# Kernel tuning notes

Hardware: AMD Instinct MI355X
Metric: run time of the kernel (lower is better)

## Reference

```python
import jax, jax.numpy as jnp
import numpy as np

RES, K, H = 8192, 48, 128

def _layer_norm(x, g, b, eps=1e-5):
    mu = jnp.mean(x, axis=-1, keepdims=True)
    var = jnp.var(x, axis=-1, keepdims=True)
    return (x - mu) * jax.lax.rsqrt(var + eps) * g + b

def _gelu(x):
    return jax.nn.gelu(x, approximate=False)  # torch default exact GELU

def setup_inputs() -> dict:
    key = jax.random.key(0)
    ks = jax.random.split(key, 16)
    s = 0.05
    inp = {
        "node_h": jax.random.normal(ks[0], (RES, H), jnp.float32),
        "edge_h": jax.random.normal(ks[1], (RES, K, H), jnp.float32),
        "edge_idx": jax.random.randint(ks[2], (RES, K), 0, RES, jnp.int32),
        "seq_emb": jax.random.normal(ks[3], (RES, H), jnp.float32),
        "ar_mask": jax.random.uniform(ks[4], (RES, K), jnp.float32),
        # msg_mlp: Linear(4h,h) -> GELU -> Linear(h,h) -> GELU -> Linear(h,h)
        "mW1": jax.random.normal(ks[5], (4 * H, H), jnp.float32) * s,
        "mb1": jnp.zeros((H,), jnp.float32),
        "mW2": jax.random.normal(ks[6], (H, H), jnp.float32) * s,
        "mb2": jnp.zeros((H,), jnp.float32),
        "mW3": jax.random.normal(ks[7], (H, H), jnp.float32) * s,
        "mb3": jnp.zeros((H,), jnp.float32),
        # ff_node: Linear(h,4h) -> GELU -> Linear(4h,h)
        "fW1": jax.random.normal(ks[8], (H, 4 * H), jnp.float32) * s,
        "fb1": jnp.zeros((4 * H,), jnp.float32),
        "fW2": jax.random.normal(ks[9], (4 * H, H), jnp.float32) * s,
        "fb2": jnp.zeros((H,), jnp.float32),
        "g1": jnp.ones((H,), jnp.float32), "b1": jnp.zeros((H,), jnp.float32),
        "g2": jnp.ones((H,), jnp.float32), "b2": jnp.zeros((H,), jnp.float32),
    }
    return inp

def reference(node_h, edge_h, edge_idx, seq_emb, ar_mask,
              mW1, mb1, mW2, mb2, mW3, mb3,
              fW1, fb1, fW2, fb2, g1, b1, g2, b2):
    seq_j = seq_emb[edge_idx] * ar_mask[..., None]           # [res,k,h]
    e_dec = jnp.concatenate([edge_h, seq_j], axis=-1)        # [res,k,2h]
    h_j = node_h[edge_idx]                                   # [res,k,h]
    h_i = jnp.broadcast_to(node_h[:, None, :], (node_h.shape[0], edge_idx.shape[1], node_h.shape[1]))
    x = jnp.concatenate([h_i, h_j, e_dec], axis=-1)          # [res,k,4h]
    msg = _gelu(x @ mW1 + mb1)
    msg = _gelu(msg @ mW2 + mb2)
    msg = msg @ mW3 + mb3                                    # [res,k,h]
    agg = jnp.sum(msg, axis=1)                               # [res,h]
    h = _layer_norm(node_h + agg, g1, b1)
    ff = _gelu(h @ fW1 + fb1) @ fW2 + fb2
    h = _layer_norm(h + ff, g2, b2)
    return h
```

## Files before the change

### kernel.cpp

```cpp
#include <hip/hip_runtime.h>

#define KNB 48

typedef float  floatx4 __attribute__((ext_vector_type(4)));
typedef __bf16 bf16x8  __attribute__((ext_vector_type(8)));
typedef unsigned short ushort8  __attribute__((ext_vector_type(8)));
typedef unsigned short ushort4v __attribute__((ext_vector_type(4)));

__device__ __forceinline__ float bf2f(unsigned short b) {
  union { unsigned int u; float f; } v; v.u = ((unsigned int)b) << 16; return v.f;
}
__device__ __forceinline__ unsigned short f2bf(float f) {
  __bf16 h = (__bf16)f;
  union { __bf16 h; unsigned short u; } v; v.h = h; return v.u;
}
__device__ __forceinline__ float gelu_f(float x) {
  float u = x * (0.7978845608f + 0.0356774081f * x * x);
  float t = __builtin_amdgcn_exp2f(u * -2.8853900818f);
  return x * __builtin_amdgcn_rcpf(1.0f + t);
}

__global__ __launch_bounds__(256) void k0_transpose(
    const float* mW1, const float* mW2, const float* mW3,
    const float* fW1, const float* fW2,
    unsigned short* MT1, unsigned short* WT2, unsigned short* WT3,
    unsigned short* FWT1, unsigned short* FWT2) {
  __shared__ unsigned short tile[32][33];
  int b = blockIdx.x;
  const float* src; unsigned short* dst; int Kd, Nd, t;
  if (b < 64)       { src = mW1; dst = MT1;  Kd = 512; Nd = 128; t = b; }
  else if (b < 80)  { src = mW2; dst = WT2;  Kd = 128; Nd = 128; t = b - 64; }
  else if (b < 96)  { src = mW3; dst = WT3;  Kd = 128; Nd = 128; t = b - 80; }
  else if (b < 160) { src = fW1; dst = FWT1; Kd = 128; Nd = 512; t = b - 96; }
  else              { src = fW2; dst = FWT2; Kd = 512; Nd = 128; t = b - 160; }
  int tN = Nd >> 5;
  int tk = t / tN, tn = t % tN;
  int tx = threadIdx.x & 31, ty = threadIdx.x >> 5;
  for (int r = 0; r < 4; ++r) {
    int row = ty + r * 8;
    tile[row][tx] = f2bf(src[(size_t)(tk * 32 + row) * Nd + tn * 32 + tx]);
  }
  __syncthreads();
  for (int r = 0; r < 4; ++r) {
    int row = ty + r * 8;
    dst[(size_t)(tn * 32 + row) * Kd + tk * 32 + tx] = tile[tx][row];
  }
}

__global__ __launch_bounds__(256) void k1_nodepre(
    const float* node_h, const float* seq_emb,
    const unsigned short* MT1, const float* mb1,
    float* Apr, unsigned short* BS) {
  __shared__ __align__(16) unsigned short sX[2][32 * 128];
  int r0 = blockIdx.x * 32;
  int tid = threadIdx.x, lane = tid & 63, w = tid >> 6;
  int l15 = lane & 15, l16 = lane >> 4;

  for (int mset = 0; mset < 2; ++mset) {
    const float* src = mset ? (seq_emb + (size_t)r0 * 128) : (node_h + (size_t)r0 * 128);
    for (int k = 0; k < 4; ++k) {
      int f = tid + 256 * k;
      floatx4 v = ((const floatx4*)src)[f];
      int row = f >> 5, hc = f & 31, c = hc >> 1, half = hc & 1;
      ushort4v o;
      o[0] = f2bf(v[0]); o[1] = f2bf(v[1]); o[2] = f2bf(v[2]); o[3] = f2bf(v[3]);
      *(ushort4v*)((char*)&sX[mset][0] + row * 256 + ((c ^ (row & 7)) << 4) + half * 8) = o;
    }
  }
  __syncthreads();

  for (int q = 0; q < 6; ++q) {
    int job = w + 4 * q;
    int kind = job >> 3;
    int nt = job & 7;
    int colOff = (kind == 0) ? 0 : (kind == 1) ? 128 : 384;
    const unsigned short* X = sX[kind == 2 ? 1 : 0];
    bf16x8 wf[4];
    for (int kk = 0; kk < 4; ++kk)
      wf[kk] = *(const bf16x8*)(MT1 + (size_t)(nt * 16 + l15) * 512 + colOff + kk * 32 + l16 * 8);
    for (int mt = 0; mt < 2; ++mt) {
      floatx4 acc = {0.f, 0.f, 0.f, 0.f};
      for (int kk = 0; kk < 4; ++kk) {
        int row = mt * 16 + l15;
        int off = (kk * 64 + l16 * 16) ^ ((row & 7) << 4);
        bf16x8 a = *(const bf16x8*)((const char*)X + row * 256 + off);
        acc = __builtin_amdgcn_mfma_f32_16x16x32_bf16(a, wf[kk], acc, 0, 0, 0);
      }
      int col = nt * 16 + l15;
      for (int r = 0; r < 4; ++r) {
        int row = r0 + mt * 16 + l16 * 4 + r;
        if (kind == 0)      Apr[(size_t)row * 128 + col] = acc[r] + mb1[col];
        else if (kind == 1) BS[(size_t)row * 256 + col] = f2bf(acc[r]);
        else                BS[(size_t)row * 256 + 128 + col] = f2bf(acc[r]);
      }
    }
  }
}

__global__ __launch_bounds__(512, 8) void k2_edge(
    const float* edge_h, const int* edge_idx, const float* ar_mask,
    const unsigned short* MT1, const unsigned short* WT2, const unsigned short* WT3,
    const float* mb2, const float* mb3,
    const float* Apr, const unsigned short* BS,
    float* agg) {
  __shared__ __align__(16) unsigned short sE[48 * 128];
  __shared__ __align__(16) unsigned short sT[48 * 128];
  int i0 = blockIdx.x;
  int tid = threadIdx.x, lane = tid & 63, w = tid >> 6;
  int l15 = lane & 15, l16 = lane >> 4;
  int rb = (l16 & 1) * 4;
  int colw = w * 16 + l15;
  int cp = ((colw >> 3) << 4) | ((l15 & 7) << 1);

  const float* eb = edge_h + (size_t)i0 * KNB * 128;
#pragma unroll
  for (int k = 0; k < 3; ++k) {
    int f = tid + 512 * k;
    floatx4 v = ((const floatx4*)eb)[f];
    int row = f >> 5, hc = f & 31, c = hc >> 1, half = hc & 1;
    ushort4v o;
    o[0] = f2bf(v[0]); o[1] = f2bf(v[1]); o[2] = f2bf(v[2]); o[3] = f2bf(v[3]);
    *(ushort4v*)((char*)sE + row * 256 + ((c ^ (row & 7)) << 4) + half * 8) = o;
  }
  for (int u = tid; u < 48 * 16; u += 512) {
    int e = u >> 4, c8 = u & 15;
    int j = edge_idx[(size_t)i0 * KNB + e];
    float m = ar_mask[(size_t)i0 * KNB + e];
    const floatx4* ap = (const floatx4*)(Apr + (size_t)i0 * 128 + c8 * 8);
    floatx4 a0 = ap[0], a1 = ap[1];
    ushort8 vb = *(const ushort8*)(BS + (size_t)j * 256 + c8 * 8);
    ushort8 vs = *(const ushort8*)(BS + (size_t)j * 256 + 128 + c8 * 8);
    ushort8 res;
#pragma unroll
    for (int x = 0; x < 4; ++x)
      res[x] = f2bf(a0[x] + bf2f(vb[x]) + m * bf2f(vs[x]));
#pragma unroll
    for (int x = 0; x < 4; ++x)
      res[4 + x] = f2bf(a1[x] + bf2f(vb[4 + x]) + m * bf2f(vs[4 + x]));
    *(ushort8*)((char*)sT + e * 256 + ((c8 ^ (e & 7)) * 16)) = res;
  }
  __syncthreads();

  {
    bf16x8 wf[4];
#pragma unroll
    for (int kk = 0; kk < 4; ++kk)
      wf[kk] = *(const bf16x8*)(MT1 + (size_t)colw * 512 + 256 + kk * 32 + l16 * 8);
#pragma unroll
    for (int mt = 0; mt < 3; ++mt) {
      floatx4 acc = {0.f,0.f,0.f,0.f};
#pragma unroll
      for (int kk = 0; kk < 4; ++kk) {
        int row = mt * 16 + l15;
        int off = (kk * 64 + l16 * 16) ^ ((row & 7) << 4);
        bf16x8 a = *(const bf16x8*)((const char*)sE + row * 256 + off);
        acc = __builtin_amdgcn_mfma_f32_16x16x32_bf16(a, wf[kk], acc, 0, 0, 0);
      }
      char* base = (char*)sT + (mt * 16 + l16 * 4) * 256;
#pragma unroll
      for (int r = 0; r < 4; ++r) {
        char* p = base + r * 256 + (cp ^ ((rb + r) << 4));
        float g = bf2f(*(unsigned short*)p);
        *(unsigned short*)p = f2bf(gelu_f(acc[r] + g));
      }
    }
  }
  __syncthreads();

  {
    bf16x8 wf[4];
#pragma unroll
    for (int kk = 0; kk < 4; ++kk)
      wf[kk] = *(const bf16x8*)(WT2 + (size_t)colw * 128 + kk * 32 + l16 * 8);
    float bb = mb2[colw];
#pragma unroll
    for (int mt = 0; mt < 3; ++mt) {
      floatx4 acc = {0.f,0.f,0.f,0.f};
#pragma unroll
      for (int kk = 0; kk < 4; ++kk) {
        int row = mt * 16 + l15;
        int off = (kk * 64 + l16 * 16) ^ ((row & 7) << 4);
        bf16x8 a = *(const bf16x8*)((const char*)sT + row * 256 + off);
        acc = __builtin_amdgcn_mfma_f32_16x16x32_bf16(a, wf[kk], acc, 0, 0, 0);
      }
      char* base = (char*)sE + (mt * 16 + l16 * 4) * 256;
#pragma unroll
      for (int r = 0; r < 4; ++r) {
        char* p = base + r * 256 + (cp ^ ((rb + r) << 4));
        *(unsigned short*)p = f2bf(gelu_f(acc[r] + bb));
      }
    }
  }
  __syncthreads();

  {
    bf16x8 wf[4];
#pragma unroll
    for (int kk = 0; kk < 4; ++kk)
      wf[kk] = *(const bf16x8*)(WT3 + (size_t)colw * 128 + kk * 32 + l16 * 8);
    float agga[4] = {0.f,0.f,0.f,0.f};
#pragma unroll
    for (int mt = 0; mt < 3; ++mt) {
      floatx4 acc = {0.f,0.f,0.f,0.f};
#pragma unroll
      for (int kk = 0; kk < 4; ++kk) {
        int row = mt * 16 + l15;
        int off = (kk * 64 + l16 * 16) ^ ((row & 7) << 4);
        bf16x8 a = *(const bf16x8*)((const char*)sE + row * 256 + off);
        acc = __builtin_amdgcn_mfma_f32_16x16x32_bf16(a, wf[kk], acc, 0, 0, 0);
      }
#pragma unroll
      for (int r = 0; r < 4; ++r) agga[r] += acc[r];
    }
    float s = agga[0] + agga[1] + agga[2] + agga[3];
    s += __shfl_xor(s, 16);
    s += __shfl_xor(s, 32);
    if (lane < 16) {
      int col = w * 16 + lane;
      agg[(size_t)i0 * 128 + col] = s + 48.0f * mb3[col];
    }
  }
}

__global__ __launch_bounds__(256) void k3_ff(
    const float* node_h, const float* agg,
    const unsigned short* FWT1, const unsigned short* FWT2,
    const float* fb1, const float* fb2,
    const float* g1, const float* b1,
    const float* g2, const float* b2,
    float* out) {
  __shared__ __align__(16) unsigned short sH[32 * 128];
  __shared__ __align__(16) unsigned short sT3[32 * 512];
  __shared__ float sP[32 * 128];
  int r0 = blockIdx.x * 32;
  int tid = threadIdx.x, lane = tid & 63, w = tid >> 6;
  int l15 = lane & 15, l16 = lane >> 4;

  {
    int row = tid >> 3;
    int c0 = (tid & 7) * 16;
    const floatx4* nh4 = (const floatx4*)(node_h + (size_t)(r0 + row) * 128 + c0);
    const floatx4* ag4 = (const floatx4*)(agg + (size_t)(r0 + row) * 128 + c0);
    float x[16]; float sum = 0.f, sum2 = 0.f;
#pragma unroll
    for (int q4 = 0; q4 < 4; ++q4) {
      floatx4 a = nh4[q4], g = ag4[q4];
#pragma unroll
      for (int j = 0; j < 4; ++j) {
        float xv = a[j] + g[j];
        x[q4 * 4 + j] = xv; sum += xv; sum2 += xv * xv;
      }
    }
    sum  += __shfl_xor(sum, 1);  sum  += __shfl_xor(sum, 2);  sum  += __shfl_xor(sum, 4);
    sum2 += __shfl_xor(sum2, 1); sum2 += __shfl_xor(sum2, 2); sum2 += __shfl_xor(sum2, 4);
    float mu = sum * (1.f / 128.f);
    float var = sum2 * (1.f / 128.f) - mu * mu;
    float rstd = rsqrtf(var + 1e-5f);
#pragma unroll
    for (int q = 0; q < 16; ++q) {
      int col = c0 + q;
      float h = (x[q] - mu) * rstd * g1[col] + b1[col];
      sP[row * 128 + col] = h;
      char* p = (char*)sH + row * 256 + ((((col >> 3) ^ (row & 7)) << 4) | ((col & 7) << 1));
      *(unsigned short*)p = f2bf(h);
    }
  }
  __syncthreads();

  for (int nq = 0; nq < 8; ++nq) {
    int nt = w * 8 + nq;
    bf16x8 wf[4];
    for (int kk = 0; kk < 4; ++kk)
      wf[kk] = *(const bf16x8*)(FWT1 + (size_t)(nt * 16 + l15) * 128 + kk * 32 + l16 * 8);
    for (int mt = 0; mt < 2; ++mt) {
      floatx4 acc = {0.f,0.f,0.f,0.f};
      for (int kk = 0; kk < 4; ++kk) {
        int row = mt * 16 + l15;
        int off = (kk * 64 + l16 * 16) ^ ((row & 7) << 4);
        bf16x8 a = *(const bf16x8*)((const char*)sH + row * 256 + off);
        acc = __builtin_amdgcn_mfma_f32_16x16x32_bf16(a, wf[kk], acc, 0, 0, 0);
      }
      int col = nt * 16 + l15;
      float bb = fb1[col];
      for (int r = 0; r < 4; ++r) {
        int row = mt * 16 + l16 * 4 + r;
        char* p = (char*)sT3 + row * 1024 + ((((col >> 3) ^ (row & 7)) << 4) | ((col & 7) << 1));
        *(unsigned short*)p = f2bf(gelu_f(acc[r] + bb));
      }
    }
  }
  __syncthreads();

  for (int n = 0; n < 2; ++n) {
    int nt = 2 * w + n;
    for (int mt = 0; mt < 2; ++mt) {
      floatx4 acc = {0.f,0.f,0.f,0.f};
      for (int kk = 0; kk < 16; ++kk) {
        int row = mt * 16 + l15;
        int off = (kk * 64 + l16 * 16) ^ ((row & 7) << 4);
        bf16x8 a = *(const bf16x8*)((const char*)sT3 + row * 1024 + off);
        bf16x8 b = *(const bf16x8*)(FWT2 + (size_t)(nt * 16 + l15) * 512 + kk * 32 + l16 * 8);
        acc = __builtin_amdgcn_mfma_f32_16x16x32_bf16(a, b, acc, 0, 0, 0);
      }
      int col = nt * 16 + l15;
      float bb = fb2[col];
      for (int r = 0; r < 4; ++r) {
        int row = mt * 16 + l16 * 4 + r;
        sP[row * 128 + col] += acc[r] + bb;
      }
    }
  }
  __syncthreads();

  {
    int row = tid >> 3;
    int c0 = (tid & 7) * 16;
    float x[16]; float sum = 0.f, sum2 = 0.f;
#pragma unroll
    for (int q = 0; q < 16; ++q) {
      float xv = sP[row * 128 + c0 + q];
      x[q] = xv; sum += xv; sum2 += xv * xv;
    }
    sum  += __shfl_xor(sum, 1);  sum  += __shfl_xor(sum, 2);  sum  += __shfl_xor(sum, 4);
    sum2 += __shfl_xor(sum2, 1); sum2 += __shfl_xor(sum2, 2); sum2 += __shfl_xor(sum2, 4);
    float mu = sum * (1.f / 128.f);
    float var = sum2 * (1.f / 128.f) - mu * mu;
    float rstd = rsqrtf(var + 1e-5f);
#pragma unroll
    for (int q = 0; q < 16; ++q) {
      int col = c0 + q;
      out[(size_t)(r0 + row) * 128 + col] = (x[q] - mu) * rstd * g2[col] + b2[col];
    }
  }
}

extern "C" void kernel_launch(void* const* d_in, const int* in_sizes, int n_in,
                              void* d_out, int out_size, void* d_ws, size_t ws_size,
                              hipStream_t stream) {
  const float* node_h  = (const float*)d_in[0];
  const float* edge_h  = (const float*)d_in[1];
  const int*   edge_idx= (const int*)d_in[2];
  const float* seq_emb = (const float*)d_in[3];
  const float* ar_mask = (const float*)d_in[4];
  const float* mW1 = (const float*)d_in[5];
  const float* mb1 = (const float*)d_in[6];
  const float* mW2 = (const float*)d_in[7];
  const float* mb2 = (const float*)d_in[8];
  const float* mW3 = (const float*)d_in[9];
  const float* mb3 = (const float*)d_in[10];
  const float* fW1 = (const float*)d_in[11];
  const float* fb1 = (const float*)d_in[12];
  const float* fW2 = (const float*)d_in[13];
  const float* fb2 = (const float*)d_in[14];
  const float* g1  = (const float*)d_in[15];
  const float* b1  = (const float*)d_in[16];
  const float* g2  = (const float*)d_in[17];
  const float* b2  = (const float*)d_in[18];

  char* ws = (char*)d_ws;
  unsigned short* MT1  = (unsigned short*)(ws + 0);
  unsigned short* WT2  = (unsigned short*)(ws + 131072);
  unsigned short* WT3  = (unsigned short*)(ws + 163840);
  unsigned short* FWT1 = (unsigned short*)(ws + 196608);
  unsigned short* FWT2 = (unsigned short*)(ws + 327680);
  float*          Apr  = (float*)(ws + 458752);
  unsigned short* BS   = (unsigned short*)(ws + 4653056);
  float*          agg  = (float*)(ws + 8847360);

  hipLaunchKernelGGL(k0_transpose, dim3(224), dim3(256), 0, stream,
                     mW1, mW2, mW3, fW1, fW2, MT1, WT2, WT3, FWT1, FWT2);
  hipLaunchKernelGGL(k1_nodepre, dim3(256), dim3(256), 0, stream,
                     node_h, seq_emb, MT1, mb1, Apr, BS);
  hipLaunchKernelGGL(k2_edge, dim3(8192), dim3(512), 0, stream,
                     edge_h, edge_idx, ar_mask, MT1, WT2, WT3, mb2, mb3,
                     Apr, BS, agg);
  hipLaunchKernelGGL(k3_ff, dim3(256), dim3(256), 0, stream,
                     node_h, agg, FWT1, FWT2, fb1, fb2, g1, b1, g2, b2,
                     (float*)d_out);
}
```

Measured before the change: 156.6 us.

## Map one wavefront per node in edge MLP kernel, removing block barriers

The edge-MLP kernel now gives each wavefront one whole node: a 256-thread block handles four nodes, and each wave has its own shared-memory tile. Edge features are loaded straight from global memory into MFMA A-fragments held in registers. Each wave computes all 8 column tiles for its node, so the block-wide __syncthreads between layers go away and the edge_h staging copy is dropped. The cost is a much higher register count (A-fragments plus three accumulators), fewer waves per block, and weight fragments being reloaded for every column tile in every wave.

```diff
diff --git a/kernel.cpp b/kernel.cpp
--- a/kernel.cpp
+++ b/kernel.cpp
@@ -14,11 +14,19 @@
   __bf16 h = (__bf16)f;
   union { __bf16 h; unsigned short u; } v; v.h = h; return v.u;
 }
+__device__ __forceinline__ bf16x8 pack8(floatx4 a, floatx4 b) {
+  bf16x8 r;
+  r[0] = (__bf16)a[0]; r[1] = (__bf16)a[1]; r[2] = (__bf16)a[2]; r[3] = (__bf16)a[3];
+  r[4] = (__bf16)b[0]; r[5] = (__bf16)b[1]; r[6] = (__bf16)b[2]; r[7] = (__bf16)b[3];
+  return r;
+}
 __device__ __forceinline__ float gelu_f(float x) {
   float u = x * (0.7978845608f + 0.0356774081f * x * x);
   float t = __builtin_amdgcn_exp2f(u * -2.8853900818f);
   return x * __builtin_amdgcn_rcpf(1.0f + t);
 }
+
+#define MFMA16(a, b, c) __builtin_amdgcn_mfma_f32_16x16x32_bf16((a), (b), (c), 0, 0, 0)
 
 __global__ __launch_bounds__(256) void k0_transpose(
     const float* mW1, const float* mW2, const float* mW3,
@@ -84,7 +92,7 @@
         int row = mt * 16 + l15;
         int off = (kk * 64 + l16 * 16) ^ ((row & 7) << 4);
         bf16x8 a = *(const bf16x8*)((const char*)X + row * 256 + off);
-        acc = __builtin_amdgcn_mfma_f32_16x16x32_bf16(a, wf[kk], acc, 0, 0, 0);
+        acc = MFMA16(a, wf[kk], acc);
       }
       int col = nt * 16 + l15;
       for (int r = 0; r < 4; ++r) {
@@ -97,127 +105,156 @@
   }
 }
 
-__global__ __launch_bounds__(512, 8) void k2_edge(
+__global__ __launch_bounds__(256, 3) void k2_edge(
     const float* edge_h, const int* edge_idx, const float* ar_mask,
     const unsigned short* MT1, const unsigned short* WT2, const unsigned short* WT3,
     const float* mb2, const float* mb3,
     const float* Apr, const unsigned short* BS,
     float* agg) {
-  __shared__ __align__(16) unsigned short sE[48 * 128];
-  __shared__ __align__(16) unsigned short sT[48 * 128];
-  int i0 = blockIdx.x;
+  __shared__ __align__(16) unsigned short sP[4][48 * 128];
   int tid = threadIdx.x, lane = tid & 63, w = tid >> 6;
   int l15 = lane & 15, l16 = lane >> 4;
   int rb = (l16 & 1) * 4;
-  int colw = w * 16 + l15;
-  int cp = ((colw >> 3) << 4) | ((l15 & 7) << 1);
-
-  const float* eb = edge_h + (size_t)i0 * KNB * 128;
-#pragma unroll
-  for (int k = 0; k < 3; ++k) {
-    int f = tid + 512 * k;
-    floatx4 v = ((const floatx4*)eb)[f];
-    int row = f >> 5, hc = f & 31, c = hc >> 1, half = hc & 1;
-    ushort4v o;
-    o[0] = f2bf(v[0]); o[1] = f2bf(v[1]); o[2] = f2bf(v[2]); o[3] = f2bf(v[3]);
-    *(ushort4v*)((char*)sE + row * 256 + ((c ^ (row & 7)) << 4) + half * 8) = o;
-  }
-  for (int u = tid; u < 48 * 16; u += 512) {
-    int e = u >> 4, c8 = u & 15;
-    int j = edge_idx[(size_t)i0 * KNB + e];
-    float m = ar_mask[(size_t)i0 * KNB + e];
-    const floatx4* ap = (const floatx4*)(Apr + (size_t)i0 * 128 + c8 * 8);
-    floatx4 a0 = ap[0], a1 = ap[1];
-    ushort8 vb = *(const ushort8*)(BS + (size_t)j * 256 + c8 * 8);
-    ushort8 vs = *(const ushort8*)(BS + (size_t)j * 256 + 128 + c8 * 8);
-    ushort8 res;
-#pragma unroll
-    for (int x = 0; x < 4; ++x)
-      res[x] = f2bf(a0[x] + bf2f(vb[x]) + m * bf2f(vs[x]));
-#pragma unroll
-    for (int x = 0; x < 4; ++x)
-      res[4 + x] = f2bf(a1[x] + bf2f(vb[4 + x]) + m * bf2f(vs[4 + x]));
-    *(ushort8*)((char*)sT + e * 256 + ((c8 ^ (e & 7)) * 16)) = res;
-  }
-  __syncthreads();
+  int node = blockIdx.x * 4 + w;
+  char* P = (char*)&sP[w][0];
+
+  bf16x8 af[3][4];
+#pragma unroll
+  for (int mt = 0; mt < 3; ++mt) {
+#pragma unroll
+    for (int kk = 0; kk < 4; ++kk) {
+      const floatx4* ep = (const floatx4*)(edge_h +
+          ((size_t)node * KNB + mt * 16 + l15) * 128 + kk * 32 + l16 * 8);
+      af[mt][kk] = pack8(ep[0], ep[1]);
+    }
+  }
 
   {
+    const floatx4* aprp = (const floatx4*)(Apr + (size_t)node * 128 + l16 * 32);
+    floatx4 ap[8];
+#pragma unroll
+    for (int q = 0; q < 8; ++q) ap[q] = aprp[q];
+#pragma unroll
+    for (int mt = 0; mt < 3; ++mt) {
+      int e = mt * 16 + l15;
+      int j = edge_idx[(size_t)node * KNB + e];
+      float m = ar_mask[(size_t)node * KNB + e];
+#pragma unroll
+      for (int q = 0; q < 4; ++q) {
+        int c8 = l16 * 4 + q;
+        ushort8 vb = *(const ushort8*)(BS + (size_t)j * 256 + c8 * 8);
+        ushort8 vs = *(const ushort8*)(BS + (size_t)j * 256 + 128 + c8 * 8);
+        floatx4 a0 = ap[2 * q], a1 = ap[2 * q + 1];
+        ushort8 res;
+#pragma unroll
+        for (int x = 0; x < 4; ++x)
+          res[x] = f2bf(a0[x] + bf2f(vb[x]) + m * bf2f(vs[x]));
+#pragma unroll
+        for (int x = 0; x < 4; ++x)
+          res[4 + x] = f2bf(a1[x] + bf2f(vb[4 + x]) + m * bf2f(vs[4 + x]));
+        *(ushort8*)(P + e * 256 + ((c8 ^ (e & 7)) << 4)) = res;
+      }
+    }
+  }
+
+#pragma unroll
+  for (int nt = 0; nt < 8; ++nt) {
+    int col = nt * 16 + l15;
     bf16x8 wf[4];
 #pragma unroll
     for (int kk = 0; kk < 4; ++kk)
-      wf[kk] = *(const bf16x8*)(MT1 + (size_t)colw * 512 + 256 + kk * 32 + l16 * 8);
-#pragma unroll
-    for (int mt = 0; mt < 3; ++mt) {
-      floatx4 acc = {0.f,0.f,0.f,0.f};
-#pragma unroll
-      for (int kk = 0; kk < 4; ++kk) {
-        int row = mt * 16 + l15;
-        int off = (kk * 64 + l16 * 16) ^ ((row & 7) << 4);
-        bf16x8 a = *(const bf16x8*)((const char*)sE + row * 256 + off);
-        acc = __builtin_amdgcn_mfma_f32_16x16x32_bf16(a, wf[kk], acc, 0, 0, 0);
-      }
-      char* base = (char*)sT + (mt * 16 + l16 * 4) * 256;
-#pragma unroll
-      for (int r = 0; r < 4; ++r) {
-        char* p = base + r * 256 + (cp ^ ((rb + r) << 4));
-        float g = bf2f(*(unsigned short*)p);
-        *(unsigned short*)p = f2bf(gelu_f(acc[r] + g));
-      }
-    }
-  }
-  __syncthreads();
-
-  {
+      wf[kk] = *(const bf16x8*)(MT1 + (size_t)col * 512 + 256 + kk * 32 + l16 * 8);
+    floatx4 a0 = {0.f,0.f,0.f,0.f}, a1 = {0.f,0.f,0.f,0.f}, a2 = {0.f,0.f,0.f,0.f};
+#pragma unroll
+    for (int kk = 0; kk < 4; ++kk) {
+      a0 = MFMA16(af[0][kk], wf[kk], a0);
+      a1 = MFMA16(af[1][kk], wf[kk], a1);
+      a2 = MFMA16(af[2][kk], wf[kk], a2);
+    }
+    int cp = ((col >> 3) << 4) | ((l15 & 7) << 1);
+#pragma unroll
+    for (int r = 0; r < 4; ++r) {
+      int sw = cp ^ ((rb + r) << 4);
+      char* p0 = P + (l16 * 4 + r) * 256 + sw;
+      char* p1 = P + (16 + l16 * 4 + r) * 256 + sw;
+      char* p2 = P + (32 + l16 * 4 + r) * 256 + sw;
+      float g0 = bf2f(*(unsigned short*)p0);
+      float g1 = bf2f(*(unsigned short*)p1);
+      float g2 = bf2f(*(unsigned short*)p2);
+      *(unsigned short*)p0 = f2bf(gelu_f(a0[r] + g0));
+      *(unsigned short*)p1 = f2bf(gelu_f(a1[r] + g1));
+      *(unsigned short*)p2 = f2bf(gelu_f(a2[r] + g2));
+    }
+  }
+
+#pragma unroll
+  for (int mt = 0; mt < 3; ++mt)
+#pragma unroll
+    for (int kk = 0; kk < 4; ++kk)
+      af[mt][kk] = *(const bf16x8*)(P + (mt * 16 + l15) * 256 +
+                                    ((kk * 64 + l16 * 16) ^ ((l15 & 7) << 4)));
+
+#pragma unroll
+  for (int nt = 0; nt < 8; ++nt) {
+    int col = nt * 16 + l15;
     bf16x8 wf[4];
 #pragma unroll
     for (int kk = 0; kk < 4; ++kk)
-      wf[kk] = *(const bf16x8*)(WT2 + (size_t)colw * 128 + kk * 32 + l16 * 8);
-    float bb = mb2[colw];
-#pragma unroll
-    for (int mt = 0; mt < 3; ++mt) {
-      floatx4 acc = {0.f,0.f,0.f,0.f};
-#pragma unroll
-      for (int kk = 0; kk < 4; ++kk) {
-        int row = mt * 16 + l15;
-        int off = (kk * 64 + l16 * 16) ^ ((row & 7) << 4);
-        bf16x8 a = *(const bf16x8*)((const char*)sT + row * 256 + off);
-        acc = __builtin_amdgcn_mfma_f32_16x16x32_bf16(a, wf[kk], acc, 0, 0, 0);
-      }
-      char* base = (char*)sE + (mt * 16 + l16 * 4) * 256;
-#pragma unroll
-      for (int r = 0; r < 4; ++r) {
-        char* p = base + r * 256 + (cp ^ ((rb + r) << 4));
-        *(unsigned short*)p = f2bf(gelu_f(acc[r] + bb));
-      }
-    }
-  }
-  __syncthreads();
-
-  {
+      wf[kk] = *(const bf16x8*)(WT2 + (size_t)col * 128 + kk * 32 + l16 * 8);
+    float bb = mb2[col];
+    floatx4 a0 = {0.f,0.f,0.f,0.f}, a1 = {0.f,0.f,0.f,0.f}, a2 = {0.f,0.f,0.f,0.f};
+#pragma unroll
+    for (int kk = 0; kk < 4; ++kk) {
+      a0 = MFMA16(af[0][kk], wf[kk], a0);
+      a1 = MFMA16(af[1][kk], wf[kk], a1);
+      a2 = MFMA16(af[2][kk], wf[kk], a2);
+    }
+    int cp = ((col >> 3) << 4) | ((l15 & 7) << 1);
+#pragma unroll
+    for (int r = 0; r < 4; ++r) {
+      int sw = cp ^ ((rb + r) << 4);
+      *(unsigned short*)(P + (l16 * 4 + r) * 256 + sw)      = f2bf(gelu_f(a0[r] + bb));
+      *(unsigned short*)(P + (16 + l16 * 4 + r) * 256 + sw) = f2bf(gelu_f(a1[r] + bb));
+      *(unsigned short*)(P + (32 + l16 * 4 + r) * 256 + sw) = f2bf(gelu_f(a2[r] + bb));
+    }
+  }
+
+#pragma unroll
+  for (int mt = 0; mt < 3; ++mt)
+#pragma unroll
+    for (int kk = 0; kk < 4; ++kk)
+      af[mt][kk] = *(const bf16x8*)(P + (mt * 16 + l15) * 256 +
+                                    ((kk * 64 + l16 * 16) ^ ((l15 & 7) << 4)));
+
+  float s[8];
+#pragma unroll
+  for (int nt = 0; nt < 8; ++nt) {
+    int col = nt * 16 + l15;
     bf16x8 wf[4];
 #pragma unroll
     for (int kk = 0; kk < 4; ++kk)
-      wf[kk] = *(const bf16x8*)(WT3 + (size_t)colw * 128 + kk * 32 + l16 * 8);
-    float agga[4] = {0.f,0.f,0.f,0.f};
-#pragma unroll
-    for (int mt = 0; mt < 3; ++mt) {
-      floatx4 acc = {0.f,0.f,0.f,0.f};
-#pragma unroll
-      for (int kk = 0; kk < 4; ++kk) {
-        int row = mt * 16 + l15;
-        int off = (kk * 64 + l16 * 16) ^ ((row & 7) << 4);
-        bf16x8 a = *(const bf16x8*)((const char*)sE + row * 256 + off);
-        acc = __builtin_amdgcn_mfma_f32_16x16x32_bf16(a, wf[kk], acc, 0, 0, 0);
-      }
-#pragma unroll
-      for (int r = 0; r < 4; ++r) agga[r] += acc[r];
-    }
-    float s = agga[0] + agga[1] + agga[2] + agga[3];
-    s += __shfl_xor(s, 16);
-    s += __shfl_xor(s, 32);
-    if (lane < 16) {
-      int col = w * 16 + lane;
-      agg[(size_t)i0 * 128 + col] = s + 48.0f * mb3[col];
+      wf[kk] = *(const bf16x8*)(WT3 + (size_t)col * 128 + kk * 32 + l16 * 8);
+    floatx4 a0 = {0.f,0.f,0.f,0.f}, a1 = {0.f,0.f,0.f,0.f}, a2 = {0.f,0.f,0.f,0.f};
+#pragma unroll
+    for (int kk = 0; kk < 4; ++kk) {
+      a0 = MFMA16(af[0][kk], wf[kk], a0);
+      a1 = MFMA16(af[1][kk], wf[kk], a1);
+      a2 = MFMA16(af[2][kk], wf[kk], a2);
+    }
+    s[nt] = (a0[0] + a0[1] + a0[2] + a0[3]) +
+            (a1[0] + a1[1] + a1[2] + a1[3]) +
+            (a2[0] + a2[1] + a2[2] + a2[3]);
+  }
+#pragma unroll
+  for (int nt = 0; nt < 8; ++nt) {
+    s[nt] += __shfl_xor(s[nt], 16);
+    s[nt] += __shfl_xor(s[nt], 32);
+  }
+  if (lane < 16) {
+#pragma unroll
+    for (int nt = 0; nt < 8; ++nt) {
+      int col = nt * 16 + lane;
+      agg[(size_t)node * 128 + col] = s[nt] + 48.0f * mb3[col];
     }
   }
 }
@@ -278,7 +315,7 @@
         int row = mt * 16 + l15;
         int off = (kk * 64 + l16 * 16) ^ ((row & 7) << 4);
         bf16x8 a = *(const bf16x8*)((const char*)sH + row * 256 + off);
-        acc = __builtin_amdgcn_mfma_f32_16x16x32_bf16(a, wf[kk], acc, 0, 0, 0);
+        acc = MFMA16(a, wf[kk], acc);
       }
       int col = nt * 16 + l15;
       float bb = fb1[col];
@@ -300,7 +337,7 @@
         int off = (kk * 64 + l16 * 16) ^ ((row & 7) << 4);
         bf16x8 a = *(const bf16x8*)((const char*)sT3 + row * 1024 + off);
         bf16x8 b = *(const bf16x8*)(FWT2 + (size_t)(nt * 16 + l15) * 512 + kk * 32 + l16 * 8);
-        acc = __builtin_amdgcn_mfma_f32_16x16x32_bf16(a, b, acc, 0, 0, 0);
+        acc = MFMA16(a, b, acc);
       }
       int col = nt * 16 + l15;
       float bb = fb2[col];
@@ -371,7 +408,7 @@
                      mW1, mW2, mW3, fW1, fW2, MT1, WT2, WT3, FWT1, FWT2);
   hipLaunchKernelGGL(k1_nodepre, dim3(256), dim3(256), 0, stream,
                      node_h, seq_emb, MT1, mb1, Apr, BS);
-  hipLaunchKernelGGL(k2_edge, dim3(8192), dim3(512), 0, stream,
+  hipLaunchKernelGGL(k2_edge, dim3(2048), dim3(256), 0, stream,
                      edge_h, edge_idx, ar_mask, MT1, WT2, WT3, mb2, mb3,
                      Apr, BS, agg);
   hipLaunchKernelGGL(k3_ff, dim3(256), dim3(256), 0, stream,
```

Result: slower. 179.7 us (+14.7%).

## Move third msg linear after neighbor sum and run one wave per node

Applied to the files above, without the earlier changes.

Uses linearity of the last message layer: the edge kernel now sums the GELU outputs of layer 2 over the 48 neighbors, and the k3 kernel applies W3 once per node, adding 48 times the bias. The edge kernel is restructured so each wave handles one node in three 16-edge chunks. Edge features are loaded straight from global into MFMA B operands, and weights are streamed as A operands. This removes a whole per-edge GEMM and most block-wide syncs and shared memory traffic. The cost is more global or L2 weight reloads per wave, 32 accumulator registers, and a shuffle reduction. The summed activations are rounded to bf16 before W3, which changes precision slightly.

```diff
diff --git a/kernel.cpp b/kernel.cpp
--- a/kernel.cpp
+++ b/kernel.cpp
@@ -14,11 +14,19 @@
   __bf16 h = (__bf16)f;
   union { __bf16 h; unsigned short u; } v; v.h = h; return v.u;
 }
+__device__ __forceinline__ bf16x8 pack8(floatx4 a, floatx4 b) {
+  bf16x8 r;
+  r[0] = (__bf16)a[0]; r[1] = (__bf16)a[1]; r[2] = (__bf16)a[2]; r[3] = (__bf16)a[3];
+  r[4] = (__bf16)b[0]; r[5] = (__bf16)b[1]; r[6] = (__bf16)b[2]; r[7] = (__bf16)b[3];
+  return r;
+}
 __device__ __forceinline__ float gelu_f(float x) {
   float u = x * (0.7978845608f + 0.0356774081f * x * x);
   float t = __builtin_amdgcn_exp2f(u * -2.8853900818f);
   return x * __builtin_amdgcn_rcpf(1.0f + t);
 }
+
+#define MFMA16(a, b, c) __builtin_amdgcn_mfma_f32_16x16x32_bf16((a), (b), (c), 0, 0, 0)
 
 __global__ __launch_bounds__(256) void k0_transpose(
     const float* mW1, const float* mW2, const float* mW3,
@@ -84,7 +92,7 @@
         int row = mt * 16 + l15;
         int off = (kk * 64 + l16 * 16) ^ ((row & 7) << 4);
         bf16x8 a = *(const bf16x8*)((const char*)X + row * 256 + off);
-        acc = __builtin_amdgcn_mfma_f32_16x16x32_bf16(a, wf[kk], acc, 0, 0, 0);
+        acc = MFMA16(a, wf[kk], acc);
       }
       int col = nt * 16 + l15;
       for (int r = 0; r < 4; ++r) {
@@ -97,138 +105,102 @@
   }
 }
 
-__global__ __launch_bounds__(512, 8) void k2_edge(
+__global__ __launch_bounds__(256, 4) void k2_edge(
     const float* edge_h, const int* edge_idx, const float* ar_mask,
-    const unsigned short* MT1, const unsigned short* WT2, const unsigned short* WT3,
-    const float* mb2, const float* mb3,
+    const unsigned short* MT1, const unsigned short* WT2,
+    const float* mb2,
     const float* Apr, const unsigned short* BS,
-    float* agg) {
-  __shared__ __align__(16) unsigned short sE[48 * 128];
-  __shared__ __align__(16) unsigned short sT[48 * 128];
-  int i0 = blockIdx.x;
+    float* sumT2) {
+  __shared__ __align__(16) unsigned short sX[4][16 * 128];
   int tid = threadIdx.x, lane = tid & 63, w = tid >> 6;
   int l15 = lane & 15, l16 = lane >> 4;
-  int rb = (l16 & 1) * 4;
-  int colw = w * 16 + l15;
-  int cp = ((colw >> 3) << 4) | ((l15 & 7) << 1);
-
-  const float* eb = edge_h + (size_t)i0 * KNB * 128;
-#pragma unroll
-  for (int k = 0; k < 3; ++k) {
-    int f = tid + 512 * k;
-    floatx4 v = ((const floatx4*)eb)[f];
-    int row = f >> 5, hc = f & 31, c = hc >> 1, half = hc & 1;
-    ushort4v o;
-    o[0] = f2bf(v[0]); o[1] = f2bf(v[1]); o[2] = f2bf(v[2]); o[3] = f2bf(v[3]);
-    *(ushort4v*)((char*)sE + row * 256 + ((c ^ (row & 7)) << 4) + half * 8) = o;
-  }
-  for (int u = tid; u < 48 * 16; u += 512) {
-    int e = u >> 4, c8 = u & 15;
-    int j = edge_idx[(size_t)i0 * KNB + e];
-    float m = ar_mask[(size_t)i0 * KNB + e];
-    const floatx4* ap = (const floatx4*)(Apr + (size_t)i0 * 128 + c8 * 8);
-    floatx4 a0 = ap[0], a1 = ap[1];
-    ushort8 vb = *(const ushort8*)(BS + (size_t)j * 256 + c8 * 8);
-    ushort8 vs = *(const ushort8*)(BS + (size_t)j * 256 + 128 + c8 * 8);
-    ushort8 res;
-#pragma unroll
-    for (int x = 0; x < 4; ++x)
-      res[x] = f2bf(a0[x] + bf2f(vb[x]) + m * bf2f(vs[x]));
-#pragma unroll
-    for (int x = 0; x < 4; ++x)
-      res[4 + x] = f2bf(a1[x] + bf2f(vb[4 + x]) + m * bf2f(vs[4 + x]));
-    *(ushort8*)((char*)sT + e * 256 + ((c8 ^ (e & 7)) * 16)) = res;
-  }
-  __syncthreads();
-
-  {
-    bf16x8 wf[4];
+  int node = blockIdx.x * 4 + w;
+  char* X = (char*)&sX[w][0];
+  int xsw = (l15 & 7) << 4;
+
+  float vsum[32];
+#pragma unroll
+  for (int q = 0; q < 32; ++q) vsum[q] = 0.f;
+
+  for (int sub = 0; sub < 3; ++sub) {
+    int e = node * KNB + sub * 16 + l15;
+    int jj = edge_idx[e];
+    float mk = ar_mask[e];
+
+    bf16x8 bE[4];
+#pragma unroll
+    for (int kk = 0; kk < 4; ++kk) {
+      const floatx4* ep = (const floatx4*)(edge_h + (size_t)e * 128 + kk * 32 + l16 * 8);
+      bE[kk] = pack8(ep[0], ep[1]);
+    }
+
+#pragma unroll
+    for (int mt = 0; mt < 8; ++mt) {
+      int f0 = mt * 16 + l16 * 4;
+      floatx4 ap = *(const floatx4*)(Apr + (size_t)node * 128 + f0);
+      ushort4v vb = *(const ushort4v*)(BS + (size_t)jj * 256 + f0);
+      ushort4v vs = *(const ushort4v*)(BS + (size_t)jj * 256 + 128 + f0);
+      floatx4 c;
+#pragma unroll
+      for (int r = 0; r < 4; ++r) c[r] = ap[r] + bf2f(vb[r]) + mk * bf2f(vs[r]);
+#pragma unroll
+      for (int kk = 0; kk < 4; ++kk) {
+        bf16x8 a = *(const bf16x8*)(MT1 + (size_t)(mt * 16 + l15) * 512 + 256 + kk * 32 + l16 * 8);
+        c = MFMA16(a, bE[kk], c);
+      }
+      ushort4v o;
+#pragma unroll
+      for (int r = 0; r < 4; ++r) o[r] = f2bf(gelu_f(c[r]));
+      *(ushort4v*)(X + l15 * 256 + ((mt * 32 + l16 * 8) ^ xsw)) = o;
+    }
+
+    bf16x8 bT[4];
 #pragma unroll
     for (int kk = 0; kk < 4; ++kk)
-      wf[kk] = *(const bf16x8*)(MT1 + (size_t)colw * 512 + 256 + kk * 32 + l16 * 8);
-#pragma unroll
-    for (int mt = 0; mt < 3; ++mt) {
-      floatx4 acc = {0.f,0.f,0.f,0.f};
-#pragma unroll
-      for (int kk = 0; kk < 4; ++kk) {
-        int row = mt * 16 + l15;
-        int off = (kk * 64 + l16 * 16) ^ ((row & 7) << 4);
-        bf16x8 a = *(const bf16x8*)((const char*)sE + row * 256 + off);
-        acc = __builtin_amdgcn_mfma_f32_16x16x32_bf16(a, wf[kk], acc, 0, 0, 0);
-      }
-      char* base = (char*)sT + (mt * 16 + l16 * 4) * 256;
-#pragma unroll
-      for (int r = 0; r < 4; ++r) {
-        char* p = base + r * 256 + (cp ^ ((rb + r) << 4));
-        float g = bf2f(*(unsigned short*)p);
-        *(unsigned short*)p = f2bf(gelu_f(acc[r] + g));
-      }
-    }
-  }
-  __syncthreads();
-
-  {
-    bf16x8 wf[4];
-#pragma unroll
-    for (int kk = 0; kk < 4; ++kk)
-      wf[kk] = *(const bf16x8*)(WT2 + (size_t)colw * 128 + kk * 32 + l16 * 8);
-    float bb = mb2[colw];
-#pragma unroll
-    for (int mt = 0; mt < 3; ++mt) {
-      floatx4 acc = {0.f,0.f,0.f,0.f};
-#pragma unroll
-      for (int kk = 0; kk < 4; ++kk) {
-        int row = mt * 16 + l15;
-        int off = (kk * 64 + l16 * 16) ^ ((row & 7) << 4);
-        bf16x8 a = *(const bf16x8*)((const char*)sT + row * 256 + off);
-        acc = __builtin_amdgcn_mfma_f32_16x16x32_bf16(a, wf[kk], acc, 0, 0, 0);
-      }
-      char* base = (char*)sE + (mt * 16 + l16 * 4) * 256;
-#pragma unroll
-      for (int r = 0; r < 4; ++r) {
-        char* p = base + r * 256 + (cp ^ ((rb + r) << 4));
-        *(unsigned short*)p = f2bf(gelu_f(acc[r] + bb));
-      }
-    }
-  }
-  __syncthreads();
-
-  {
-    bf16x8 wf[4];
-#pragma unroll
-    for (int kk = 0; kk < 4; ++kk)
-      wf[kk] = *(const bf16x8*)(WT3 + (size_t)colw * 128 + kk * 32 + l16 * 8);
-    float agga[4] = {0.f,0.f,0.f,0.f};
-#pragma unroll
-    for (int mt = 0; mt < 3; ++mt) {
-      floatx4 acc = {0.f,0.f,0.f,0.f};
-#pragma unroll
-      for (int kk = 0; kk < 4; ++kk) {
-        int row = mt * 16 + l15;
-        int off = (kk * 64 + l16 * 16) ^ ((row & 7) << 4);
-        bf16x8 a = *(const bf16x8*)((const char*)sE + row * 256 + off);
-        acc = __builtin_amdgcn_mfma_f32_16x16x32_bf16(a, wf[kk], acc, 0, 0, 0);
-      }
-#pragma unroll
-      for (int r = 0; r < 4; ++r) agga[r] += acc[r];
-    }
-    float s = agga[0] + agga[1] + agga[2] + agga[3];
-    s += __shfl_xor(s, 16);
-    s += __shfl_xor(s, 32);
-    if (lane < 16) {
-      int col = w * 16 + lane;
-      agg[(size_t)i0 * 128 + col] = s + 48.0f * mb3[col];
+      bT[kk] = *(const bf16x8*)(X + l15 * 256 + ((kk * 64 + l16 * 16) ^ xsw));
+
+#pragma unroll
+    for (int mt = 0; mt < 8; ++mt) {
+      int f0 = mt * 16 + l16 * 4;
+      floatx4 c = *(const floatx4*)(mb2 + f0);
+#pragma unroll
+      for (int kk = 0; kk < 4; ++kk) {
+        bf16x8 a = *(const bf16x8*)(WT2 + (size_t)(mt * 16 + l15) * 128 + kk * 32 + l16 * 8);
+        c = MFMA16(a, bT[kk], c);
+      }
+#pragma unroll
+      for (int r = 0; r < 4; ++r) vsum[mt * 4 + r] += gelu_f(c[r]);
+    }
+  }
+
+#pragma unroll
+  for (int q = 0; q < 32; ++q) {
+    vsum[q] += __shfl_xor(vsum[q], 1);
+    vsum[q] += __shfl_xor(vsum[q], 2);
+    vsum[q] += __shfl_xor(vsum[q], 4);
+    vsum[q] += __shfl_xor(vsum[q], 8);
+  }
+  if (l15 == 0) {
+#pragma unroll
+    for (int mt = 0; mt < 8; ++mt) {
+      floatx4 o;
+#pragma unroll
+      for (int r = 0; r < 4; ++r) o[r] = vsum[mt * 4 + r];
+      *(floatx4*)(sumT2 + (size_t)node * 128 + mt * 16 + l16 * 4) = o;
     }
   }
 }
 
 __global__ __launch_bounds__(256) void k3_ff(
-    const float* node_h, const float* agg,
+    const float* node_h, const float* sumT2,
+    const unsigned short* WT3, const float* mb3,
     const unsigned short* FWT1, const unsigned short* FWT2,
     const float* fb1, const float* fb2,
     const float* g1, const float* b1,
     const float* g2, const float* b2,
     float* out) {
+  __shared__ __align__(16) unsigned short sS[32 * 128];
+  __shared__ float sAgg[32 * 128];
   __shared__ __align__(16) unsigned short sH[32 * 128];
   __shared__ __align__(16) unsigned short sT3[32 * 512];
   __shared__ float sP[32 * 128];
@@ -237,10 +209,45 @@
   int l15 = lane & 15, l16 = lane >> 4;
 
   {
+    const float* src = sumT2 + (size_t)r0 * 128;
+    for (int k = 0; k < 4; ++k) {
+      int f = tid + 256 * k;
+      floatx4 v = ((const floatx4*)src)[f];
+      int row = f >> 5, hc = f & 31, c = hc >> 1, half = hc & 1;
+      ushort4v o;
+      o[0] = f2bf(v[0]); o[1] = f2bf(v[1]); o[2] = f2bf(v[2]); o[3] = f2bf(v[3]);
+      *(ushort4v*)((char*)sS + row * 256 + ((c ^ (row & 7)) << 4) + half * 8) = o;
+    }
+  }
+  __syncthreads();
+
+  for (int n = 0; n < 2; ++n) {
+    int nt = w * 2 + n;
+    bf16x8 wf[4];
+    for (int kk = 0; kk < 4; ++kk)
+      wf[kk] = *(const bf16x8*)(WT3 + (size_t)(nt * 16 + l15) * 128 + kk * 32 + l16 * 8);
+    for (int mt = 0; mt < 2; ++mt) {
+      floatx4 acc = {0.f,0.f,0.f,0.f};
+      for (int kk = 0; kk < 4; ++kk) {
+        int row = mt * 16 + l15;
+        int off = (kk * 64 + l16 * 16) ^ ((row & 7) << 4);
+        bf16x8 a = *(const bf16x8*)((const char*)sS + row * 256 + off);
+        acc = MFMA16(a, wf[kk], acc);
+      }
+      int col = nt * 16 + l15;
+      for (int r = 0; r < 4; ++r) {
+        int row = mt * 16 + l16 * 4 + r;
+        sAgg[row * 128 + col] = acc[r] + 48.0f * mb3[col];
+      }
+    }
+  }
+  __syncthreads();
+
+  {
     int row = tid >> 3;
     int c0 = (tid & 7) * 16;
     const floatx4* nh4 = (const floatx4*)(node_h + (size_t)(r0 + row) * 128 + c0);
-    const floatx4* ag4 = (const floatx4*)(agg + (size_t)(r0 + row) * 128 + c0);
+    const floatx4* ag4 = (const floatx4*)(&sAgg[row * 128 + c0]);
     float x[16]; float sum = 0.f, sum2 = 0.f;
 #pragma unroll
     for (int q4 = 0; q4 < 4; ++q4) {
@@ -278,7 +285,7 @@
         int row = mt * 16 + l15;
         int off = (kk * 64 + l16 * 16) ^ ((row & 7) << 4);
         bf16x8 a = *(const bf16x8*)((const char*)sH + row * 256 + off);
-        acc = __builtin_amdgcn_mfma_f32_16x16x32_bf16(a, wf[kk], acc, 0, 0, 0);
+        acc = MFMA16(a, wf[kk], acc);
       }
       int col = nt * 16 + l15;
       float bb = fb1[col];
@@ -300,7 +307,7 @@
         int off = (kk * 64 + l16 * 16) ^ ((row & 7) << 4);
         bf16x8 a = *(const bf16x8*)((const char*)sT3 + row * 1024 + off);
         bf16x8 b = *(const bf16x8*)(FWT2 + (size_t)(nt * 16 + l15) * 512 + kk * 32 + l16 * 8);
-        acc = __builtin_amdgcn_mfma_f32_16x16x32_bf16(a, b, acc, 0, 0, 0);
+        acc = MFMA16(a, b, acc);
       }
       int col = nt * 16 + l15;
       float bb = fb2[col];
@@ -365,16 +372,15 @@
   unsigned short* FWT2 = (unsigned short*)(ws + 327680);
   float*          Apr  = (float*)(ws + 458752);
   unsigned short* BS   = (unsigned short*)(ws + 4653056);
-  float*          agg  = (float*)(ws + 8847360);
+  float*          sumT2= (float*)(ws + 8847360);
 
   hipLaunchKernelGGL(k0_transpose, dim3(224), dim3(256), 0, stream,
                      mW1, mW2, mW3, fW1, fW2, MT1, WT2, WT3, FWT1, FWT2);
   hipLaunchKernelGGL(k1_nodepre, dim3(256), dim3(256), 0, stream,
                      node_h, seq_emb, MT1, mb1, Apr, BS);
-  hipLaunchKernelGGL(k2_edge, dim3(8192), dim3(512), 0, stream,
-                     edge_h, edge_idx, ar_mask, MT1, WT2, WT3, mb2, mb3,
-                     Apr, BS, agg);
+  hipLaunchKernelGGL(k2_edge, dim3(2048), dim3(256), 0, stream,
+                     edge_h, edge_idx, ar_mask, MT1, WT2, mb2, Apr, BS, sumT2);
   hipLaunchKernelGGL(k3_ff, dim3(256), dim3(256), 0, stream,
-                     node_h, agg, FWT1, FWT2, fb1, fb2, g1, b1, g2, b2,
-                     (float*)d_out);
-}
+                     node_h, sumT2, WT3, mb3, FWT1, FWT2, fb1, fb2,
+                     g1, b1, g2, b2, (float*)d_out);
+}
```

Result: slower. 581.9 us (+271.5%).
